# Kernel optimization log

Measured on AMD Instinct MI355X. Metric: run time of the kernel, lower is better.

Reference implementation:

```python
import jax, jax.numpy as jnp
import numpy as np

V = 50000
E = 10000
Q = 32
F_DIM = 256
OUT_DIM = 256
B = 2


def setup_inputs() -> dict:
    key = jax.random.key(0)
    k1, k2, k3, k4 = jax.random.split(key, 4)
    X = jax.random.normal(k1, (B, V, F_DIM), dtype=jnp.float32)
    edge_nodes = jax.random.randint(k2, (E, Q), 0, V, dtype=jnp.int64)
    W = jax.random.normal(k3, (OUT_DIM, F_DIM), dtype=jnp.float32) * (1.0 / np.sqrt(F_DIM))
    b = jax.random.normal(k4, (OUT_DIM,), dtype=jnp.float32) * 0.01
    return {"X": X, "edge_nodes": edge_nodes, "W": W, "b": b}


def reference(X, edge_nodes, W, b):
    # X: [B, V, F]; edge_nodes: [E, Q] node indices per hyperedge
    Bn, Vn, Fn = X.shape
    En, Qn = edge_nodes.shape
    # gather-mean per hyperedge: agg[b,e,:] = mean_q X[b, edge_nodes[e,q], :]
    gathered = X[:, edge_nodes, :]                      # [B, E, Q, F]
    agg = gathered.mean(axis=2)                          # [B, E, F]
    flat = edge_nodes.reshape(-1)                        # [E*Q]
    # scatter-add agg back to every member node of its hyperedge
    vals = jnp.broadcast_to(agg[:, :, None, :], (Bn, En, Qn, Fn)).reshape(Bn, En * Qn, Fn)
    X_out = jnp.zeros_like(X).at[:, flat, :].add(vals)   # [B, V, F]
    # degree = number of hyperedge memberships per node, clamped to >= 1
    deg = jnp.zeros((Vn,), X.dtype).at[flat].add(1.0)
    deg = jnp.maximum(deg, 1.0)
    X_out = X_out / deg[None, :, None]
    # fc: Linear(in_dim, out_dim)
    return X_out @ W.T + b
```

## Files before the change

### kernel.cpp

```cpp
#include <hip/hip_runtime.h>
#include <hip/hip_bf16.h>
#include <stdint.h>

static constexpr int V_N = 50000;
static constexpr int E_N = 10000;
static constexpr int Q_N = 32;
static constexpr int F_N = 256;
static constexpr int SLOT_STRIDE = 40;
static constexpr int VF4 = V_N * F_N / 4;
static constexpr int NXV = 2 * VF4;
static constexpr int NWV = (F_N * F_N) / 4;
static constexpr int T_TILES = E_N / 8;
static constexpr int LDS_STRIDE = 264;

static constexpr int PREP_GRID = 2048;
static constexpr int XBLK = 1536;
static constexpr int XNT = XBLK * 256;
static constexpr int WBLK = 16;
static constexpr int BBLK = 512 - WBLK;

typedef unsigned short us;
typedef float f32x4 __attribute__((ext_vector_type(4)));
typedef us us4 __attribute__((ext_vector_type(4)));
typedef us us8 __attribute__((ext_vector_type(8)));
typedef __bf16 bf16x8 __attribute__((ext_vector_type(8)));

__device__ __forceinline__ us f2b(float f) {
  unsigned x = __builtin_bit_cast(unsigned, f);
  x += 0x7fffu + ((x >> 16) & 1u);
  return (us)(x >> 16);
}
__device__ __forceinline__ float b2f(us u) {
  unsigned x = ((unsigned)u) << 16;
  return __builtin_bit_cast(float, x);
}

__device__ __forceinline__ int xidx(int i) {
  int b = (i >= VF4) ? 1 : 0;
  int r2 = i - b * VF4;
  return ((r2 >> 6) << 7) + (b << 6) + (r2 & 63);
}


__global__ __launch_bounds__(256) void k_prep_bucket(
    const float* __restrict__ X, const float* __restrict__ Wm,
    const int* __restrict__ en, us* __restrict__ Xb, us* __restrict__ Wb,
    int* __restrict__ cnt, int* __restrict__ slots) {
  const int bx = blockIdx.x;
  const int r = bx & 3;
  if (r != 3) {
    const int tid = ((bx >> 2) * 3 + r) * 256 + (int)threadIdx.x;
    int i = tid;
    for (; i + 3 * XNT < NXV; i += 4 * XNT) {
      f32x4 va = ((const f32x4*)X)[i];
      f32x4 vb = ((const f32x4*)X)[i + XNT];
      f32x4 vc = ((const f32x4*)X)[i + 2 * XNT];
      f32x4 vd = ((const f32x4*)X)[i + 3 * XNT];
      us4 oa, ob, oc, od;
      #pragma unroll
      for (int j = 0; j < 4; ++j) {
        oa[j] = f2b(va[j]); ob[j] = f2b(vb[j]);
        oc[j] = f2b(vc[j]); od[j] = f2b(vd[j]);
      }
      ((us4*)Xb)[xidx(i)] = oa;
      ((us4*)Xb)[xidx(i + XNT)] = ob;
      ((us4*)Xb)[xidx(i + 2 * XNT)] = oc;
      ((us4*)Xb)[xidx(i + 3 * XNT)] = od;
    }
    for (; i < NXV; i += XNT) {
      f32x4 v = ((const f32x4*)X)[i];
      us4 o;
      #pragma unroll
      for (int j = 0; j < 4; ++j) o[j] = f2b(v[j]);
      ((us4*)Xb)[xidx(i)] = o;
    }
  } else {
    const int s = bx >> 2;
    if (s < WBLK) {
      const int tid = s * 256 + (int)threadIdx.x;
      for (int i = tid; i < NWV; i += WBLK * 256) {
        f32x4 v = ((const f32x4*)Wm)[i];
        us4 o;
        #pragma unroll
        for (int j = 0; j < 4; ++j) o[j] = f2b(v[j]);
        ((us4*)Wb)[i] = o;
      }
    } else {
      const int tid = (s - WBLK) * 256 + (int)threadIdx.x;
      for (int i = tid; i < E_N * Q_N; i += BBLK * 256) {
        int v = en[i];
        int pos = atomicAdd(&cnt[v], 1);
        if (pos < SLOT_STRIDE) slots[v * SLOT_STRIDE + pos] = i >> 5;
      }
    }
  }
}


__global__ __launch_bounds__(256) void k_agg_gemm(
    const us* __restrict__ Xb, const int* __restrict__ en,
    const us* __restrict__ Wb, us* __restrict__ Yb) {
  __shared__ us tile[16 * LDS_STRIDE];
  const int t = blockIdx.x;
  const int w = threadIdx.x >> 6;
  const int lane = threadIdx.x & 63;
  const int m = lane & 15;
  const int quad = lane >> 4;
  const int half = lane >> 5;
  const int col8 = (lane & 31) * 8;

  const int e0 = t * 8 + 2 * w;
  int n0 = en[e0 * Q_N + (lane & 31)];
  int n1 = en[(e0 + 1) * Q_N + (lane & 31)];
  const us* Xg = Xb + half * F_N + col8;
  float a0[8] = {0, 0, 0, 0, 0, 0, 0, 0};
  float a1[8] = {0, 0, 0, 0, 0, 0, 0, 0};
  #pragma unroll 4
  for (int q = 0; q < Q_N; ++q) {
    int ma = __shfl(n0, q, 64);
    int mb = __shfl(n1, q, 64);
    us8 va = *(const us8*)(Xg + (size_t)ma * (2 * F_N));
    us8 vb = *(const us8*)(Xg + (size_t)mb * (2 * F_N));
    #pragma unroll
    for (int j = 0; j < 8; ++j) { a0[j] += b2f(va[j]); a1[j] += b2f(vb[j]); }
  }
  const float sc = 1.0f / 32.0f;
  us8 o0, o1;
  #pragma unroll
  for (int j = 0; j < 8; ++j) { o0[j] = f2b(a0[j] * sc); o1[j] = f2b(a1[j] * sc); }
  *(us8*)(tile + (2 * w + 8 * half) * LDS_STRIDE + col8) = o0;
  *(us8*)(tile + (2 * w + 1 + 8 * half) * LDS_STRIDE + col8) = o1;
  __syncthreads();

  bf16x8 af[8];
  #pragma unroll
  for (int kk = 0; kk < 8; ++kk)
    af[kk] = *(const bf16x8*)(tile + m * LDS_STRIDE + quad * 8 + kk * 32);
  #pragma unroll
  for (int i = 0; i < 4; ++i) {
    const int nt = w * 4 + i;
    const us* bp = Wb + (size_t)(nt * 16 + m) * F_N + quad * 8;
    f32x4 acc = {0.f, 0.f, 0.f, 0.f};
    #pragma unroll
    for (int kk = 0; kk < 8; ++kk) {
      bf16x8 bv = *(const bf16x8*)(bp + kk * 32);
      acc = __builtin_amdgcn_mfma_f32_16x16x32_bf16(af[kk], bv, acc, 0, 0, 0);
    }
    #pragma unroll
    for (int r2 = 0; r2 < 4; ++r2) {
      int dr = quad * 4 + r2;
      int e = t * 8 + (dr & 7);
      int b = dr >> 3;
      Yb[((size_t)e * 2 + b) * 256 + nt * 16 + m] = f2b(acc[r2]);
    }
  }
}


__global__ __launch_bounds__(256) void k_out(
    const us* __restrict__ Yb, const int* __restrict__ cnt,
    const int* __restrict__ slots, const float* __restrict__ bias,
    float* __restrict__ out) {
  const int w = threadIdx.x >> 6;
  const int lane = threadIdx.x & 63;
  const int v = blockIdx.x * 4 + w;
  const int half = lane >> 5;
  const int col8 = (lane & 31) * 8;
  int c = cnt[v];
  if (c > SLOT_STRIDE) c = SLOT_STRIDE;
  const int* sb = slots + (size_t)v * SLOT_STRIDE;
  const us* Yg = Yb + half * 256 + col8;
  float acc[8] = {0, 0, 0, 0, 0, 0, 0, 0};
  int j = 0;
  for (; j + 4 <= c; j += 4) {
    int ea = sb[j], eb = sb[j + 1], ec = sb[j + 2], ed = sb[j + 3];
    us8 pa = *(const us8*)(Yg + (size_t)ea * 512);
    us8 pb = *(const us8*)(Yg + (size_t)eb * 512);
    us8 pc = *(const us8*)(Yg + (size_t)ec * 512);
    us8 pd = *(const us8*)(Yg + (size_t)ed * 512);
    #pragma unroll
    for (int k = 0; k < 8; ++k)
      acc[k] += (b2f(pa[k]) + b2f(pb[k])) + (b2f(pc[k]) + b2f(pd[k]));
  }
  for (; j < c; ++j) {
    int e = sb[j];
    us8 p = *(const us8*)(Yg + (size_t)e * 512);
    #pragma unroll
    for (int k = 0; k < 8; ++k) acc[k] += b2f(p[k]);
  }
  float inv = 1.0f / (float)(c > 0 ? c : 1);
  f32x4 b0 = *(const f32x4*)(bias + col8);
  f32x4 b1 = *(const f32x4*)(bias + col8 + 4);
  f32x4 r0, r1;
  #pragma unroll
  for (int k = 0; k < 4; ++k) {
    r0[k] = b0[k] + acc[k] * inv;
    r1[k] = b1[k] + acc[4 + k] * inv;
  }
  float* op = out + ((size_t)half * V_N + v) * 256 + col8;
  __builtin_nontemporal_store(r0, (f32x4*)op);
  __builtin_nontemporal_store(r1, (f32x4*)(op + 4));
}


extern "C" void kernel_launch(void* const* d_in, const int* in_sizes, int n_in,
                              void* d_out, int out_size, void* d_ws, size_t ws_size,
                              hipStream_t stream) {
  (void)in_sizes; (void)n_in; (void)out_size; (void)ws_size;
  const float* X = (const float*)d_in[0];
  const int* en = (const int*)d_in[1];
  const float* Wm = (const float*)d_in[2];
  const float* bias = (const float*)d_in[3];
  float* out = (float*)d_out;

  char* ws = (char*)d_ws;
  int* cnt   = (int*)(ws);
  int* slots = (int*)(ws + (1u << 20));
  us*  Wb    = (us*)(ws + (10u << 20));
  us*  Yb    = (us*)(ws + (11u << 20));
  us*  Xb    = (us*)(ws + (22u << 20));

  hipMemsetAsync(cnt, 0, V_N * sizeof(int), stream);
  k_prep_bucket<<<PREP_GRID, 256, 0, stream>>>(X, Wm, en, Xb, Wb, cnt, slots);
  k_agg_gemm<<<T_TILES, 256, 0, stream>>>(Xb, en, Wb, Yb);
  k_out<<<V_N / 4, 256, 0, stream>>>(Yb, cnt, slots, bias, out);
}
```

Baseline: 291.0 us.

## Gather fp32 X directly instead of pre-converting it to bf16

Removes the full-array X conversion to an interleaved bf16 copy in the prep kernel. The aggregation kernel now gathers fp32 rows of both batches directly from X and sums them before rounding into the LDS tile. This avoids a large streaming read and write pass over X, at the cost of gathering twice as many bytes per node visit. The prep grid shrinks to handle only W conversion and bucketing.

Measured after the change: 312.4 us. 7.3% more time.

```diff
diff --git a/kernel.cpp b/kernel.cpp
--- a/kernel.cpp
+++ b/kernel.cpp
@@ -7,17 +7,14 @@
 static constexpr int Q_N = 32;
 static constexpr int F_N = 256;
 static constexpr int SLOT_STRIDE = 40;
-static constexpr int VF4 = V_N * F_N / 4;
-static constexpr int NXV = 2 * VF4;
 static constexpr int NWV = (F_N * F_N) / 4;
 static constexpr int T_TILES = E_N / 8;
 static constexpr int LDS_STRIDE = 264;
+static constexpr int VFLT = V_N * F_N;
 
-static constexpr int PREP_GRID = 2048;
-static constexpr int XBLK = 1536;
-static constexpr int XNT = XBLK * 256;
+static constexpr int PREP_GRID = 512;
 static constexpr int WBLK = 16;
-static constexpr int BBLK = 512 - WBLK;
+static constexpr int BBLK = PREP_GRID - WBLK;
 
 typedef unsigned short us;
 typedef float f32x4 __attribute__((ext_vector_type(4)));
@@ -35,70 +32,33 @@
   return __builtin_bit_cast(float, x);
 }
 
-__device__ __forceinline__ int xidx(int i) {
-  int b = (i >= VF4) ? 1 : 0;
-  int r2 = i - b * VF4;
-  return ((r2 >> 6) << 7) + (b << 6) + (r2 & 63);
-}
 
-
-__global__ __launch_bounds__(256) void k_prep_bucket(
-    const float* __restrict__ X, const float* __restrict__ Wm,
-    const int* __restrict__ en, us* __restrict__ Xb, us* __restrict__ Wb,
-    int* __restrict__ cnt, int* __restrict__ slots) {
+__global__ __launch_bounds__(256) void k_prep(
+    const float* __restrict__ Wm, const int* __restrict__ en,
+    us* __restrict__ Wb, int* __restrict__ cnt, int* __restrict__ slots) {
   const int bx = blockIdx.x;
-  const int r = bx & 3;
-  if (r != 3) {
-    const int tid = ((bx >> 2) * 3 + r) * 256 + (int)threadIdx.x;
-    int i = tid;
-    for (; i + 3 * XNT < NXV; i += 4 * XNT) {
-      f32x4 va = ((const f32x4*)X)[i];
-      f32x4 vb = ((const f32x4*)X)[i + XNT];
-      f32x4 vc = ((const f32x4*)X)[i + 2 * XNT];
-      f32x4 vd = ((const f32x4*)X)[i + 3 * XNT];
-      us4 oa, ob, oc, od;
-      #pragma unroll
-      for (int j = 0; j < 4; ++j) {
-        oa[j] = f2b(va[j]); ob[j] = f2b(vb[j]);
-        oc[j] = f2b(vc[j]); od[j] = f2b(vd[j]);
-      }
-      ((us4*)Xb)[xidx(i)] = oa;
-      ((us4*)Xb)[xidx(i + XNT)] = ob;
-      ((us4*)Xb)[xidx(i + 2 * XNT)] = oc;
-      ((us4*)Xb)[xidx(i + 3 * XNT)] = od;
-    }
-    for (; i < NXV; i += XNT) {
-      f32x4 v = ((const f32x4*)X)[i];
+  if (bx < WBLK) {
+    const int tid = bx * 256 + (int)threadIdx.x;
+    for (int i = tid; i < NWV; i += WBLK * 256) {
+      f32x4 v = ((const f32x4*)Wm)[i];
       us4 o;
       #pragma unroll
       for (int j = 0; j < 4; ++j) o[j] = f2b(v[j]);
-      ((us4*)Xb)[xidx(i)] = o;
+      ((us4*)Wb)[i] = o;
     }
   } else {
-    const int s = bx >> 2;
-    if (s < WBLK) {
-      const int tid = s * 256 + (int)threadIdx.x;
-      for (int i = tid; i < NWV; i += WBLK * 256) {
-        f32x4 v = ((const f32x4*)Wm)[i];
-        us4 o;
-        #pragma unroll
-        for (int j = 0; j < 4; ++j) o[j] = f2b(v[j]);
-        ((us4*)Wb)[i] = o;
-      }
-    } else {
-      const int tid = (s - WBLK) * 256 + (int)threadIdx.x;
-      for (int i = tid; i < E_N * Q_N; i += BBLK * 256) {
-        int v = en[i];
-        int pos = atomicAdd(&cnt[v], 1);
-        if (pos < SLOT_STRIDE) slots[v * SLOT_STRIDE + pos] = i >> 5;
-      }
+    const int tid = (bx - WBLK) * 256 + (int)threadIdx.x;
+    for (int i = tid; i < E_N * Q_N; i += BBLK * 256) {
+      int v = en[i];
+      int pos = atomicAdd(&cnt[v], 1);
+      if (pos < SLOT_STRIDE) slots[v * SLOT_STRIDE + pos] = i >> 5;
     }
   }
 }
 
 
 __global__ __launch_bounds__(256) void k_agg_gemm(
-    const us* __restrict__ Xb, const int* __restrict__ en,
+    const float* __restrict__ X, const int* __restrict__ en,
     const us* __restrict__ Wb, us* __restrict__ Yb) {
   __shared__ us tile[16 * LDS_STRIDE];
   const int t = blockIdx.x;
@@ -106,30 +66,40 @@
   const int lane = threadIdx.x & 63;
   const int m = lane & 15;
   const int quad = lane >> 4;
-  const int half = lane >> 5;
-  const int col8 = (lane & 31) * 8;
+  const int col4 = lane * 4;
 
   const int e0 = t * 8 + 2 * w;
   int n0 = en[e0 * Q_N + (lane & 31)];
   int n1 = en[(e0 + 1) * Q_N + (lane & 31)];
-  const us* Xg = Xb + half * F_N + col8;
-  float a0[8] = {0, 0, 0, 0, 0, 0, 0, 0};
-  float a1[8] = {0, 0, 0, 0, 0, 0, 0, 0};
+  const float* X0 = X + col4;
+  const float* X1 = X + (size_t)VFLT + col4;
+  float a00[4] = {0, 0, 0, 0}, a01[4] = {0, 0, 0, 0};
+  float a10[4] = {0, 0, 0, 0}, a11[4] = {0, 0, 0, 0};
   #pragma unroll 4
   for (int q = 0; q < Q_N; ++q) {
     int ma = __shfl(n0, q, 64);
     int mb = __shfl(n1, q, 64);
-    us8 va = *(const us8*)(Xg + (size_t)ma * (2 * F_N));
-    us8 vb = *(const us8*)(Xg + (size_t)mb * (2 * F_N));
+    f32x4 v0a = *(const f32x4*)(X0 + (size_t)ma * F_N);
+    f32x4 v1a = *(const f32x4*)(X1 + (size_t)ma * F_N);
+    f32x4 v0b = *(const f32x4*)(X0 + (size_t)mb * F_N);
+    f32x4 v1b = *(const f32x4*)(X1 + (size_t)mb * F_N);
     #pragma unroll
-    for (int j = 0; j < 8; ++j) { a0[j] += b2f(va[j]); a1[j] += b2f(vb[j]); }
+    for (int j = 0; j < 4; ++j) {
+      a00[j] += v0a[j]; a01[j] += v1a[j];
+      a10[j] += v0b[j]; a11[j] += v1b[j];
+    }
   }
   const float sc = 1.0f / 32.0f;
-  us8 o0, o1;
+  us4 o00, o01, o10, o11;
   #pragma unroll
-  for (int j = 0; j < 8; ++j) { o0[j] = f2b(a0[j] * sc); o1[j] = f2b(a1[j] * sc); }
-  *(us8*)(tile + (2 * w + 8 * half) * LDS_STRIDE + col8) = o0;
-  *(us8*)(tile + (2 * w + 1 + 8 * half) * LDS_STRIDE + col8) = o1;
+  for (int j = 0; j < 4; ++j) {
+    o00[j] = f2b(a00[j] * sc); o01[j] = f2b(a01[j] * sc);
+    o10[j] = f2b(a10[j] * sc); o11[j] = f2b(a11[j] * sc);
+  }
+  *(us4*)(tile + (2 * w) * LDS_STRIDE + col4) = o00;
+  *(us4*)(tile + (2 * w + 1) * LDS_STRIDE + col4) = o10;
+  *(us4*)(tile + (8 + 2 * w) * LDS_STRIDE + col4) = o01;
+  *(us4*)(tile + (8 + 2 * w + 1) * LDS_STRIDE + col4) = o11;
   __syncthreads();
 
   bf16x8 af[8];
@@ -218,10 +188,9 @@
   int* slots = (int*)(ws + (1u << 20));
   us*  Wb    = (us*)(ws + (10u << 20));
   us*  Yb    = (us*)(ws + (11u << 20));
-  us*  Xb    = (us*)(ws + (22u << 20));
 
   hipMemsetAsync(cnt, 0, V_N * sizeof(int), stream);
-  k_prep_bucket<<<PREP_GRID, 256, 0, stream>>>(X, Wm, en, Xb, Wb, cnt, slots);
-  k_agg_gemm<<<T_TILES, 256, 0, stream>>>(Xb, en, Wb, Yb);
+  k_prep<<<PREP_GRID, 256, 0, stream>>>(Wm, en, Wb, cnt, slots);
+  k_agg_gemm<<<T_TILES, 256, 0, stream>>>(X, en, Wb, Yb);
   k_out<<<V_N / 4, 256, 0, stream>>>(Yb, cnt, slots, bias, out);
 }
```
